# Optimization experiments

Measured on AMD Instinct MI355X. Metric: run time of the kernel, lower is better.

The kernel has to match this reference:

```python
import jax, jax.numpy as jnp
import numpy as np

N_NODES = 50000
W_IN = 256
W_OUT = 256
HEADS = 8
D_HEAD = W_OUT // HEADS
NUM_EDGE = 3
N_EDGES = 800000
NEG_SLOPE = 0.2


def setup_inputs() -> dict:
    key = jax.random.key(0)
    ks = jax.random.split(key, 10)
    x = jax.random.normal(ks[0], (N_NODES, W_IN), dtype=jnp.float32)
    adj = jax.random.randint(ks[1], (NUM_EDGE, 2, N_EDGES), 0, N_NODES, dtype=jnp.int64)
    sw = 1.0 / np.sqrt(W_IN)
    # Per-edge-type GATConv params, stacked on leading edge-type axis
    Ws = jax.random.normal(ks[2], (NUM_EDGE, W_IN, HEADS * D_HEAD), dtype=jnp.float32) * sw
    a_l = jax.random.normal(ks[3], (NUM_EDGE, HEADS, D_HEAD), dtype=jnp.float32) * 0.1
    a_r = jax.random.normal(ks[4], (NUM_EDGE, HEADS, D_HEAD), dtype=jnp.float32) * 0.1
    bias = jnp.zeros((NUM_EDGE, HEADS * D_HEAD), dtype=jnp.float32)
    # Semantic attention layer: Linear(w_out -> 1)
    att_w = jax.random.normal(ks[5], (W_OUT, 1), dtype=jnp.float32) * (1.0 / np.sqrt(W_OUT))
    att_b = jnp.zeros((1,), dtype=jnp.float32)
    return {"x": x, "adj": adj, "Ws": Ws, "a_l": a_l, "a_r": a_r,
            "bias": bias, "att_w": att_w, "att_b": att_b}


def _gat(x, edge_index, W, al, ar, b):
    # x: [N, W_IN]; edge_index: [2, E]; W: [W_IN, H*D]; al/ar: [H, D]; b: [H*D]
    N = x.shape[0]
    h = (x @ W).reshape(N, HEADS, D_HEAD)            # [N, H, D]
    src, dst = edge_index[0], edge_index[1]
    el = jnp.einsum('nhd,hd->nh', h, al)             # src-side scores [N, H]
    er = jnp.einsum('nhd,hd->nh', h, ar)             # dst-side scores [N, H]
    e = jax.nn.leaky_relu(el[src] + er[dst], NEG_SLOPE)   # [E, H]
    # segment softmax over incoming edges of each dst node
    m = jax.ops.segment_max(e, dst, num_segments=N)       # [N, H]
    e = jnp.exp(e - m[dst])
    s = jax.ops.segment_sum(e, dst, num_segments=N)       # [N, H]
    alpha = e / (s[dst] + 1e-9)                           # [E, H]
    out = jax.ops.segment_sum(alpha[:, :, None] * h[src], dst, num_segments=N)
    return out.reshape(N, HEADS * D_HEAD) + b             # concat heads [N, W_OUT]


def reference(x, adj, Ws, a_l, a_r, bias, att_w, att_b):
    outs = [_gat(x, adj[i], Ws[i], a_l[i], a_r[i], bias[i]) for i in range(NUM_EDGE)]
    stacked = jnp.stack(outs, axis=1)                     # [N, T, W_OUT]
    # AttentionLayer: scores = Linear(stacked) viewed as [N, 1, T]; NO softmax (faithful)
    att = (stacked @ att_w + att_b).reshape(-1, 1, NUM_EDGE)  # [N, 1, T]
    return jnp.matmul(att, stacked).squeeze(1)            # [N, W_OUT]
```

## Files before the change

kernel.cpp:

```cpp
#include <hip/hip_runtime.h>

#define N_NODES 50000
#define W_IN    256
#define W_OUT   256
#define HEADS   8
#define NUM_T   3
#define N_EDGES 800000
#define NEG_SLOPE 0.2f

#define NB      128
#define BSH     9
#define BNODES  512
#define P1_EPT  16
#define P1_CHUNK (256 * P1_EPT)
#define P1_BLOCKS ((N_EDGES + P1_CHUNK - 1) / P1_CHUNK)
#define NB_USED ((N_NODES + BNODES - 1) / BNODES)

#define MT_BLOCKS ((N_NODES + 127) / 128)
#define GATHER_BLOCKS ((N_NODES + 3) / 4)

#if defined(__has_builtin)
#if __has_builtin(__builtin_amdgcn_global_load_lds)
#define HAS_GLL 1
#endif
#endif

typedef __attribute__((ext_vector_type(8))) short bf16x8;
typedef __attribute__((ext_vector_type(4))) float f32x4;

__device__ __forceinline__ unsigned short f2b(float f) {
    unsigned u = __float_as_uint(f);
    u = (u + 0x7fffu + ((u >> 16) & 1u)) >> 16;
    return (unsigned short)u;
}
__device__ __forceinline__ float blo(unsigned u) { return __uint_as_float(u << 16); }
__device__ __forceinline__ float bhi(unsigned u) { return __uint_as_float(u & 0xffff0000u); }

__global__ __launch_bounds__(256) void convert_x(const float* __restrict__ x,
                                                 unsigned short* __restrict__ xb) {
    const size_t i = ((size_t)blockIdx.x * 256 + threadIdx.x) * 4;
    const float4 v = *(const float4*)(x + i);
    ushort4 o;
    o.x = f2b(v.x); o.y = f2b(v.y); o.z = f2b(v.z); o.w = f2b(v.w);
    *(ushort4*)(xb + i) = o;
}

__global__ __launch_bounds__(256) void convert_W(const float* __restrict__ Wsrc,
                                                 unsigned short* __restrict__ Wt) {
    const int t = blockIdx.y;
    const int gid = blockIdx.x * 256 + threadIdx.x;
    const int k = gid >> 8, n = gid & 255;
    Wt[(size_t)t * 65536 + (size_t)n * 256 + k] = f2b(Wsrc[(size_t)t * 65536 + gid]);
}

__global__ __launch_bounds__(256) void p1_hist(const int* __restrict__ adj,
                                               int* __restrict__ bucket_cnt) {
    __shared__ int lh[NB];
    const int t = blockIdx.y;
    const int tid = threadIdx.x;
    if (tid < NB) lh[tid] = 0;
    __syncthreads();

    const int* dstp = adj + (size_t)t * 2 * N_EDGES + N_EDGES;
    const int e0 = blockIdx.x * P1_CHUNK + tid * P1_EPT;
#pragma unroll
    for (int i = 0; i < P1_EPT; ++i) {
        const int e = e0 + i;
        if (e < N_EDGES) atomicAdd(&lh[dstp[e] >> BSH], 1);
    }
    __syncthreads();
    if (tid < NB && lh[tid] > 0) atomicAdd(&bucket_cnt[t * NB + tid], lh[tid]);
}

__global__ __launch_bounds__(128) void p1_scan(const int* __restrict__ bucket_cnt,
                                               int* __restrict__ bucket_ptr,
                                               int* __restrict__ bucket_cur) {
    __shared__ int s[NB];
    const int tid = threadIdx.x;
    for (int t = 0; t < NUM_T; ++t) {
        const int v = bucket_cnt[t * NB + tid];
        s[tid] = v;
        __syncthreads();
        for (int off = 1; off < NB; off <<= 1) {
            int o = (tid >= off) ? s[tid - off] : 0;
            __syncthreads();
            s[tid] += o;
            __syncthreads();
        }
        const int incl = s[tid];
        const int excl = incl - v;
        bucket_ptr[t * (NB + 1) + tid] = excl;
        bucket_cur[t * NB + tid] = excl;
        if (tid == NB - 1) bucket_ptr[t * (NB + 1) + NB] = incl;
        __syncthreads();
    }
}

__global__ __launch_bounds__(256) void p1_scatter(const int* __restrict__ adj,
                                                  int* __restrict__ bucket_cur,
                                                  uint2* __restrict__ part) {
    __shared__ int lh[NB];
    __shared__ int loff[NB];
    __shared__ int lbase[NB];
    __shared__ uint2 buf[P1_CHUNK];
    const int t = blockIdx.y;
    const int tid = threadIdx.x;
    const int lane = tid & 63;
    const int wave = tid >> 6;
    if (tid < NB) lh[tid] = 0;
    __syncthreads();

    const int* srcp = adj + (size_t)t * 2 * N_EDGES;
    const int* dstp = srcp + N_EDGES;
    const int e0 = blockIdx.x * P1_CHUNK + tid * P1_EPT;

    int es[P1_EPT], ed[P1_EPT], rk[P1_EPT];
#pragma unroll
    for (int i = 0; i < P1_EPT; ++i) {
        const int e = e0 + i;
        if (e < N_EDGES) {
            es[i] = srcp[e];
            ed[i] = dstp[e];
            rk[i] = atomicAdd(&lh[ed[i] >> BSH], 1);
        } else {
            ed[i] = -1;
        }
    }
    __syncthreads();

    if (tid < NB && lh[tid] > 0)
        lbase[tid] = atomicAdd(&bucket_cur[t * NB + tid], lh[tid]);
    if (wave == 0) {
        const int c0 = lh[lane * 2], c1 = lh[lane * 2 + 1];
        const int s = c0 + c1;
        int run = s;
        for (int off = 1; off < 64; off <<= 1) {
            const int o = __shfl_up(run, off);
            if (lane >= off) run += o;
        }
        const int base = run - s;
        loff[lane * 2] = base;
        loff[lane * 2 + 1] = base + c0;
    }
    __syncthreads();

#pragma unroll
    for (int i = 0; i < P1_EPT; ++i)
        if (ed[i] >= 0)
            buf[loff[ed[i] >> BSH] + rk[i]] =
                make_uint2((unsigned)es[i], (unsigned)ed[i]);
    __syncthreads();

    uint2* pt = part + (size_t)t * N_EDGES;
    int nvalid = N_EDGES - blockIdx.x * P1_CHUNK;
    if (nvalid > P1_CHUNK) nvalid = P1_CHUNK;
    for (int idx = tid; idx < nvalid; idx += 256) {
        const uint2 e = buf[idx];
        const int b = (int)(e.y >> BSH);
        pt[lbase[b] + (idx - loff[b])] = e;
    }
}

__global__ __launch_bounds__(256) void p2_csr(const uint2* __restrict__ part,
                                              const int* __restrict__ bucket_ptr,
                                              int* __restrict__ row_ptr_all,
                                              int* __restrict__ csr_all) {
    __shared__ int sc[BNODES];
    const int b = blockIdx.x;
    const int t = blockIdx.y;
    const int tid = threadIdx.x;
    const int lane = tid & 63;
    const int wave = tid >> 6;

    const uint2* pt = part + (size_t)t * N_EDGES;
    int* row_ptr = row_ptr_all + (size_t)t * (N_NODES + 1);
    int* csr = csr_all + (size_t)t * N_EDGES;

    const int bp0 = bucket_ptr[t * (NB + 1) + b];
    const int bp1 = bucket_ptr[t * (NB + 1) + b + 1];
    const int node0 = b * BNODES;
    int nn = N_NODES - node0; if (nn > BNODES) nn = BNODES;

    sc[tid] = 0; sc[tid + 256] = 0;
    __syncthreads();

    for (int idx = bp0 + tid; idx < bp1; idx += 256)
        atomicAdd(&sc[pt[idx].y - node0], 1);
    __syncthreads();

    if (wave == 0) {
        int v[8], ex[8];
        int s = 0;
#pragma unroll
        for (int i = 0; i < 8; ++i) { v[i] = sc[lane * 8 + i]; ex[i] = s; s += v[i]; }
        int run = s;
        for (int off = 1; off < 64; off <<= 1) {
            int o = __shfl_up(run, off);
            if (lane >= off) run += o;
        }
        const int base = run - s;
#pragma unroll
        for (int i = 0; i < 8; ++i) sc[lane * 8 + i] = base + ex[i];
    }
    __syncthreads();

    for (int i = tid; i < nn; i += 256) row_ptr[node0 + i] = bp0 + sc[i];
    if (b == NB_USED - 1 && tid == 0) row_ptr[N_NODES] = N_EDGES;
    __syncthreads();

    for (int idx = bp0 + tid; idx < bp1; idx += 256) {
        const uint2 e = pt[idx];
        const int pos = bp0 + atomicAdd(&sc[e.y - node0], 1);
        csr[pos] = (int)e.x;
    }
}

__global__ __launch_bounds__(256) void gemm_fused(const unsigned short* __restrict__ xb,
                                                  const unsigned short* __restrict__ Wt,
                                                  unsigned short* __restrict__ H) {
    __shared__ __attribute__((aligned(16))) unsigned short As[128 * 32];
    __shared__ __attribute__((aligned(16))) unsigned short Bs[128 * 32];

    const int tid  = threadIdx.x;
    const int wave = tid >> 6;
    const int lane = tid & 63;
    const int quad = lane >> 4;
    const int l16  = lane & 15;

    const int m0 = blockIdx.x * 128;
    const int n0 = blockIdx.y * 128;
    const int t  = blockIdx.z;

    const unsigned short* Bt = Wt + (size_t)t * 65536 + (size_t)n0 * W_IN;
    unsigned short* Hc = H + (size_t)t * N_NODES * W_OUT;

    const int moff = (wave >> 1) * 64;
    const int noff = (wave & 1) * 64;

    f32x4 acc[4][4] = {};

    const int srow = tid >> 2;
    const int sch  = (tid & 3) * 8;
    int ar0 = m0 + srow;       if (ar0 > N_NODES - 1) ar0 = N_NODES - 1;
    int ar1 = m0 + 64 + srow;  if (ar1 > N_NODES - 1) ar1 = N_NODES - 1;
    const unsigned short* a0p = xb + (size_t)ar0 * W_IN + sch;
    const unsigned short* a1p = xb + (size_t)ar1 * W_IN + sch;
    const unsigned short* b0p = Bt + (size_t)srow * W_IN + sch;
    const unsigned short* b1p = Bt + (size_t)(64 + srow) * W_IN + sch;
#if defined(HAS_GLL)
    const int ldso0 = wave * 64 * 8;
    const int ldso1 = (256 + wave * 64) * 8;
#endif

    for (int k0 = 0; k0 < W_IN; k0 += 32) {
#if defined(HAS_GLL)
        __builtin_amdgcn_global_load_lds(
            (const __attribute__((address_space(1))) void*)(a0p + k0),
            (__attribute__((address_space(3))) void*)(As + ldso0), 16, 0, 0);
        __builtin_amdgcn_global_load_lds(
            (const __attribute__((address_space(1))) void*)(a1p + k0),
            (__attribute__((address_space(3))) void*)(As + ldso1), 16, 0, 0);
        __builtin_amdgcn_global_load_lds(
            (const __attribute__((address_space(1))) void*)(b0p + k0),
            (__attribute__((address_space(3))) void*)(Bs + ldso0), 16, 0, 0);
        __builtin_amdgcn_global_load_lds(
            (const __attribute__((address_space(1))) void*)(b1p + k0),
            (__attribute__((address_space(3))) void*)(Bs + ldso1), 16, 0, 0);
#else
        {
            const uint4 av0 = *(const uint4*)(a0p + k0);
            const uint4 av1 = *(const uint4*)(a1p + k0);
            const uint4 bv0 = *(const uint4*)(b0p + k0);
            const uint4 bv1 = *(const uint4*)(b1p + k0);
            *(uint4*)&As[(size_t)tid * 8] = av0;
            *(uint4*)&As[2048 + (size_t)tid * 8] = av1;
            *(uint4*)&Bs[(size_t)tid * 8] = bv0;
            *(uint4*)&Bs[2048 + (size_t)tid * 8] = bv1;
        }
#endif
        __syncthreads();

        bf16x8 af[4], bfr[4];
#pragma unroll
        for (int mi = 0; mi < 4; ++mi)
            af[mi] = *(const bf16x8*)&As[(moff + mi * 16 + l16) * 32 + quad * 8];
#pragma unroll
        for (int ni = 0; ni < 4; ++ni)
            bfr[ni] = *(const bf16x8*)&Bs[(noff + ni * 16 + l16) * 32 + quad * 8];
#pragma unroll
        for (int mi = 0; mi < 4; ++mi)
#pragma unroll
            for (int ni = 0; ni < 4; ++ni)
                acc[mi][ni] = __builtin_amdgcn_mfma_f32_16x16x32_bf16(
                    af[mi], bfr[ni], acc[mi][ni], 0, 0, 0);
        __syncthreads();
    }

#pragma unroll
    for (int mi = 0; mi < 4; ++mi)
#pragma unroll
        for (int reg = 0; reg < 4; ++reg) {
            const int gr = m0 + moff + mi * 16 + quad * 4 + reg;
            if (gr < N_NODES)
#pragma unroll
                for (int ni = 0; ni < 4; ++ni)
                    Hc[(size_t)gr * W_OUT + n0 + noff + ni * 16 + l16] =
                        f2b(acc[mi][ni][reg]);
        }
}

__global__ __launch_bounds__(256) void compute_elr(
    const unsigned short* __restrict__ H, const float* __restrict__ a_l,
    const float* __restrict__ a_r, float* __restrict__ el,
    float* __restrict__ er) {
    const int node = (blockIdx.x * blockDim.x + threadIdx.x) >> 6;
    if (node >= N_NODES) return;
    const int t = blockIdx.y;
    const int lane = threadIdx.x & 63;
    const int h = lane >> 3;
    const int j8 = lane & 7;

    const size_t row = (size_t)t * N_NODES + node;
    const uint2 u = *(const uint2*)(H + row * W_OUT + h * 32 + j8 * 4);
    const float4 av = *(const float4*)(a_l + t * 256 + h * 32 + j8 * 4);
    const float4 rv = *(const float4*)(a_r + t * 256 + h * 32 + j8 * 4);
    const float c0 = blo(u.x), c1 = bhi(u.x), c2 = blo(u.y), c3 = bhi(u.y);
    float pl = c0 * av.x + c1 * av.y + c2 * av.z + c3 * av.w;
    float pr = c0 * rv.x + c1 * rv.y + c2 * rv.z + c3 * rv.w;
#pragma unroll
    for (int off = 1; off < 8; off <<= 1) {
        pl += __shfl_xor(pl, off);
        pr += __shfl_xor(pr, off);
    }
    if (j8 == 0) el[row * HEADS + h] = pl;
    if (j8 == 1) er[row * HEADS + h] = pr;
}

__device__ __forceinline__ void gather_accum(const int node, const int lane,
                                             const int* __restrict__ csr_src,
                                             const int* __restrict__ row_ptr,
                                             const float* __restrict__ el,
                                             const float* __restrict__ er,
                                             const unsigned short* __restrict__ H,
                                             float2 (&acc)[4], float& ssum) {
    const int half = lane >> 5;
    const int d8 = lane & 31;
    const int hh = d8 >> 2;

    const int beg = row_ptr[node];
    const int deg = row_ptr[node + 1] - beg;
    if (deg <= 0) return;
    const float erv = er[(size_t)node * HEADS + hh];

    int mysrc = (lane < deg) ? csr_src[beg + lane] : 0;
    const int npairs = (deg + 1) >> 1;

    int src0 = __shfl(mysrc, half);
    uint4 u0 = *(const uint4*)(H + (size_t)src0 * W_OUT + d8 * 8);
    float elv0 = el[(size_t)src0 * HEADS + hh];

    for (int q = 0; q < npairs; ++q) {
        int src1 = 0; uint4 u1 = u0; float elv1 = 0.f;
        const int q1 = q + 1;
        if (q1 < npairs) {
            if ((q1 & 31) == 0) {
                const int cb = beg + (q1 >> 5) * 64;
                mysrc = (cb + lane < beg + deg) ? csr_src[cb + lane] : 0;
            }
            src1 = __shfl(mysrc, (2 * q1 + half) & 63);
            u1 = *(const uint4*)(H + (size_t)src1 * W_OUT + d8 * 8);
            elv1 = el[(size_t)src1 * HEADS + hh];
        }
        float v = elv0 + erv;
        v = (v > 0.f) ? v : NEG_SLOPE * v;
        const float w = (2 * q + half < deg) ? __expf(v) : 0.f;
        acc[0].x += w * blo(u0.x); acc[0].y += w * bhi(u0.x);
        acc[1].x += w * blo(u0.y); acc[1].y += w * bhi(u0.y);
        acc[2].x += w * blo(u0.z); acc[2].y += w * bhi(u0.z);
        acc[3].x += w * blo(u0.w); acc[3].y += w * bhi(u0.w);
        ssum += w;
        src0 = src1; u0 = u1; elv0 = elv1;
    }
}

__global__ __launch_bounds__(256) void gat_gather_all(
    const int* __restrict__ csr_src, const int* __restrict__ row_ptr,
    const float* __restrict__ el, const float* __restrict__ er,
    const unsigned short* __restrict__ H,
    const float* __restrict__ bias, const float* __restrict__ att_w,
    const float* __restrict__ att_b, float* __restrict__ out) {
    const int node = (blockIdx.x * blockDim.x + threadIdx.x) >> 6;
    const int lane = threadIdx.x & 63;
    if (node >= N_NODES) return;

    float2 acc[NUM_T][4] = {};
    float ssum[NUM_T] = {};

#pragma unroll
    for (int t = 0; t < NUM_T; ++t)
        gather_accum(node, lane,
                     csr_src + (size_t)t * N_EDGES,
                     row_ptr + (size_t)t * (N_NODES + 1),
                     el + (size_t)t * N_NODES * HEADS,
                     er + (size_t)t * N_NODES * HEADS,
                     H + (size_t)t * N_NODES * W_OUT,
                     acc[t], ssum[t]);

#pragma unroll
    for (int t = 0; t < NUM_T; ++t) {
#pragma unroll
        for (int i = 0; i < 4; ++i) {
            acc[t][i].x += __shfl_xor(acc[t][i].x, 32);
            acc[t][i].y += __shfl_xor(acc[t][i].y, 32);
        }
        ssum[t] += __shfl_xor(ssum[t], 32);
    }

    const int half = lane >> 5;
    const int d8 = lane & 31;
    if (half == 0) {
        const float4 aw0 = *(const float4*)(att_w + d8 * 8);
        const float4 aw1 = *(const float4*)(att_w + d8 * 8 + 4);
        float h[NUM_T][8];
        float p[NUM_T];
#pragma unroll
        for (int t = 0; t < NUM_T; ++t) {
            const float inv = 1.f / (ssum[t] + 1e-9f);
            const float4 b0 = *(const float4*)(bias + t * W_OUT + d8 * 8);
            const float4 b1 = *(const float4*)(bias + t * W_OUT + d8 * 8 + 4);
            h[t][0] = acc[t][0].x * inv + b0.x;
            h[t][1] = acc[t][0].y * inv + b0.y;
            h[t][2] = acc[t][1].x * inv + b0.z;
            h[t][3] = acc[t][1].y * inv + b0.w;
            h[t][4] = acc[t][2].x * inv + b1.x;
            h[t][5] = acc[t][2].y * inv + b1.y;
            h[t][6] = acc[t][3].x * inv + b1.z;
            h[t][7] = acc[t][3].y * inv + b1.w;
            p[t] = h[t][0] * aw0.x + h[t][1] * aw0.y + h[t][2] * aw0.z +
                   h[t][3] * aw0.w + h[t][4] * aw1.x + h[t][5] * aw1.y +
                   h[t][6] * aw1.z + h[t][7] * aw1.w;
        }
#pragma unroll
        for (int off = 1; off < 32; off <<= 1) {
            p[0] += __shfl_xor(p[0], off);
            p[1] += __shfl_xor(p[1], off);
            p[2] += __shfl_xor(p[2], off);
        }
        const float ab = att_b[0];
        const float a0 = p[0] + ab, a1 = p[1] + ab, a2 = p[2] + ab;
        float4 o0, o1;
        o0.x = a0 * h[0][0] + a1 * h[1][0] + a2 * h[2][0];
        o0.y = a0 * h[0][1] + a1 * h[1][1] + a2 * h[2][1];
        o0.z = a0 * h[0][2] + a1 * h[1][2] + a2 * h[2][2];
        o0.w = a0 * h[0][3] + a1 * h[1][3] + a2 * h[2][3];
        o1.x = a0 * h[0][4] + a1 * h[1][4] + a2 * h[2][4];
        o1.y = a0 * h[0][5] + a1 * h[1][5] + a2 * h[2][5];
        o1.z = a0 * h[0][6] + a1 * h[1][6] + a2 * h[2][6];
        o1.w = a0 * h[0][7] + a1 * h[1][7] + a2 * h[2][7];
        *(float4*)(out + (size_t)node * W_OUT + d8 * 8) = o0;
        *(float4*)(out + (size_t)node * W_OUT + d8 * 8 + 4) = o1;
    }
}

extern "C" void kernel_launch(void* const* d_in, const int* in_sizes, int n_in,
                              void* d_out, int out_size, void* d_ws, size_t ws_size,
                              hipStream_t stream) {
    const float* x     = (const float*)d_in[0];
    const int*   adj   = (const int*)d_in[1];
    const float* Ws    = (const float*)d_in[2];
    const float* a_l   = (const float*)d_in[3];
    const float* a_r   = (const float*)d_in[4];
    const float* bias  = (const float*)d_in[5];
    const float* att_w = (const float*)d_in[6];
    const float* att_b = (const float*)d_in[7];
    float* out = (float*)d_out;

    char* w = (char*)d_ws;
    unsigned short* xb = (unsigned short*)w; w += (size_t)N_NODES * W_IN * 2;
    unsigned short* H  = (unsigned short*)w; w += (size_t)NUM_T * N_NODES * W_OUT * 2;
    unsigned short* Wt = (unsigned short*)w; w += (size_t)NUM_T * 65536 * 2;
    float* el = (float*)w; w += (size_t)NUM_T * N_NODES * HEADS * 4;
    float* er = (float*)w; w += (size_t)NUM_T * N_NODES * HEADS * 4;
    int* csr_src = (int*)w; w += (size_t)NUM_T * N_EDGES * 4;
    int* row_ptr = (int*)w; w += (size_t)NUM_T * (N_NODES + 1) * 4;
    int* bucket_cnt = (int*)w; w += NUM_T * NB * 4;
    int* bucket_ptr = (int*)w; w += NUM_T * (NB + 1) * 4;
    int* bucket_cur = (int*)w; w += NUM_T * NB * 4;
    uint2* part = (uint2*)H;

    hipMemsetAsync(bucket_cnt, 0, NUM_T * NB * sizeof(int), stream);
    convert_x<<<12500, 256, 0, stream>>>(x, xb);
    convert_W<<<dim3(256, NUM_T), 256, 0, stream>>>(Ws, Wt);
    p1_hist<<<dim3(P1_BLOCKS, NUM_T), 256, 0, stream>>>(adj, bucket_cnt);
    p1_scan<<<1, 128, 0, stream>>>(bucket_cnt, bucket_ptr, bucket_cur);
    p1_scatter<<<dim3(P1_BLOCKS, NUM_T), 256, 0, stream>>>(adj, bucket_cur, part);
    p2_csr<<<dim3(NB_USED, NUM_T), 256, 0, stream>>>(part, bucket_ptr, row_ptr,
                                                     csr_src);

    gemm_fused<<<dim3(MT_BLOCKS, 2, NUM_T), 256, 0, stream>>>(xb, Wt, H);

    compute_elr<<<dim3(GATHER_BLOCKS, NUM_T), 256, 0, stream>>>(H, a_l, a_r,
                                                                el, er);

    gat_gather_all<<<GATHER_BLOCKS, 256, 0, stream>>>(
        csr_src, row_ptr, el, er, H, bias, att_w, att_b, out);
}
```

Measured before the change: 462.8 us.

## Split gather into channel-half blocks with bf16 intermediate and separate combine kernel

The fused gather-plus-attention kernel is split in two. The gather kernel now handles half of the 256 channels per block, with four edge lanes per wave, and writes bf16 per-type outputs to a new workspace buffer. A separate combine kernel adds bias, computes the semantic attention scores and writes the final output. The aim is to shrink each wave's per-edge row footprint and raise parallelism and L2 locality over the channel halves. The cost is an extra kernel launch, a bf16 round-trip through global memory and some precision loss.

```diff
diff --git a/kernel.cpp b/kernel.cpp
--- a/kernel.cpp
+++ b/kernel.cpp
@@ -18,6 +18,7 @@
 
 #define MT_BLOCKS ((N_NODES + 127) / 128)
 #define GATHER_BLOCKS ((N_NODES + 3) / 4)
+#define SPLIT_BLOCKS 25000
 
 #if defined(__has_builtin)
 #if __has_builtin(__builtin_amdgcn_global_load_lds)
@@ -336,130 +337,139 @@
     if (j8 == 1) er[row * HEADS + h] = pr;
 }
 
-__device__ __forceinline__ void gather_accum(const int node, const int lane,
-                                             const int* __restrict__ csr_src,
-                                             const int* __restrict__ row_ptr,
-                                             const float* __restrict__ el,
-                                             const float* __restrict__ er,
-                                             const unsigned short* __restrict__ H,
-                                             float2 (&acc)[4], float& ssum) {
-    const int half = lane >> 5;
-    const int d8 = lane & 31;
-    const int hh = d8 >> 2;
-
-    const int beg = row_ptr[node];
-    const int deg = row_ptr[node + 1] - beg;
-    if (deg <= 0) return;
-    const float erv = er[(size_t)node * HEADS + hh];
-
-    int mysrc = (lane < deg) ? csr_src[beg + lane] : 0;
-    const int npairs = (deg + 1) >> 1;
-
-    int src0 = __shfl(mysrc, half);
-    uint4 u0 = *(const uint4*)(H + (size_t)src0 * W_OUT + d8 * 8);
-    float elv0 = el[(size_t)src0 * HEADS + hh];
-
-    for (int q = 0; q < npairs; ++q) {
-        int src1 = 0; uint4 u1 = u0; float elv1 = 0.f;
-        const int q1 = q + 1;
-        if (q1 < npairs) {
-            if ((q1 & 31) == 0) {
-                const int cb = beg + (q1 >> 5) * 64;
-                mysrc = (cb + lane < beg + deg) ? csr_src[cb + lane] : 0;
-            }
-            src1 = __shfl(mysrc, (2 * q1 + half) & 63);
-            u1 = *(const uint4*)(H + (size_t)src1 * W_OUT + d8 * 8);
-            elv1 = el[(size_t)src1 * HEADS + hh];
-        }
-        float v = elv0 + erv;
-        v = (v > 0.f) ? v : NEG_SLOPE * v;
-        const float w = (2 * q + half < deg) ? __expf(v) : 0.f;
-        acc[0].x += w * blo(u0.x); acc[0].y += w * bhi(u0.x);
-        acc[1].x += w * blo(u0.y); acc[1].y += w * bhi(u0.y);
-        acc[2].x += w * blo(u0.z); acc[2].y += w * bhi(u0.z);
-        acc[3].x += w * blo(u0.w); acc[3].y += w * bhi(u0.w);
-        ssum += w;
-        src0 = src1; u0 = u1; elv0 = elv1;
-    }
-}
-
-__global__ __launch_bounds__(256) void gat_gather_all(
+__global__ __launch_bounds__(256) void gat_gather_split(
     const int* __restrict__ csr_src, const int* __restrict__ row_ptr,
     const float* __restrict__ el, const float* __restrict__ er,
-    const unsigned short* __restrict__ H,
-    const float* __restrict__ bias, const float* __restrict__ att_w,
-    const float* __restrict__ att_b, float* __restrict__ out) {
-    const int node = (blockIdx.x * blockDim.x + threadIdx.x) >> 6;
+    const unsigned short* __restrict__ H, unsigned short* __restrict__ ot) {
+    const int bid = blockIdx.x;
+    const int q   = bid >> 3;
+    const int r   = bid & 7;
+    const int ch  = r >> 2;
+    const int sub = r & 3;
+    const int node = (q * 4 + sub) * 4 + (threadIdx.x >> 6);
+    if (node >= N_NODES) return;
     const int lane = threadIdx.x & 63;
-    if (node >= N_NODES) return;
+    const int g    = lane >> 4;
+    const int d16  = lane & 15;
+    const int hh   = ch * 4 + (d16 >> 2);
+    const int cbase = ch * 128 + d16 * 8;
 
     float2 acc[NUM_T][4] = {};
     float ssum[NUM_T] = {};
 
 #pragma unroll
-    for (int t = 0; t < NUM_T; ++t)
-        gather_accum(node, lane,
-                     csr_src + (size_t)t * N_EDGES,
-                     row_ptr + (size_t)t * (N_NODES + 1),
-                     el + (size_t)t * N_NODES * HEADS,
-                     er + (size_t)t * N_NODES * HEADS,
-                     H + (size_t)t * N_NODES * W_OUT,
-                     acc[t], ssum[t]);
-
-#pragma unroll
     for (int t = 0; t < NUM_T; ++t) {
+        const int* cs = csr_src + (size_t)t * N_EDGES;
+        const int* rp = row_ptr + (size_t)t * (N_NODES + 1);
+        const float* elc = el + (size_t)t * N_NODES * HEADS;
+        const float* erc = er + (size_t)t * N_NODES * HEADS;
+        const unsigned short* Hc = H + (size_t)t * N_NODES * W_OUT;
+
+        const int beg = rp[node];
+        const int deg = rp[node + 1] - beg;
+        if (deg <= 0) continue;
+        const float erv = erc[(size_t)node * HEADS + hh];
+
+        int mysrc = (lane < deg) ? cs[beg + lane] : 0;
+        const int nq = (deg + 3) >> 2;
+
+        int s0 = __shfl(mysrc, g);
+        uint4 u0 = *(const uint4*)(Hc + (size_t)s0 * W_OUT + cbase);
+        float e0 = elc[(size_t)s0 * HEADS + hh];
+
+        for (int qd = 0; qd < nq; ++qd) {
+            int s1 = 0; uint4 u1 = u0; float e1 = 0.f;
+            const int q1 = qd + 1;
+            if (q1 < nq) {
+                if ((q1 & 15) == 0) {
+                    const int base = beg + (q1 >> 4) * 64;
+                    mysrc = (base + lane < beg + deg) ? cs[base + lane] : 0;
+                }
+                s1 = __shfl(mysrc, (4 * q1 + g) & 63);
+                u1 = *(const uint4*)(Hc + (size_t)s1 * W_OUT + cbase);
+                e1 = elc[(size_t)s1 * HEADS + hh];
+            }
+            float v = e0 + erv;
+            v = (v > 0.f) ? v : NEG_SLOPE * v;
+            const float w = (4 * qd + g < deg) ? __expf(v) : 0.f;
+            acc[t][0].x += w * blo(u0.x); acc[t][0].y += w * bhi(u0.x);
+            acc[t][1].x += w * blo(u0.y); acc[t][1].y += w * bhi(u0.y);
+            acc[t][2].x += w * blo(u0.z); acc[t][2].y += w * bhi(u0.z);
+            acc[t][3].x += w * blo(u0.w); acc[t][3].y += w * bhi(u0.w);
+            ssum[t] += w;
+            s0 = s1; u0 = u1; e0 = e1;
+        }
+    }
+
+#pragma unroll
+    for (int t = 0; t < NUM_T; ++t) {
 #pragma unroll
         for (int i = 0; i < 4; ++i) {
+            acc[t][i].x += __shfl_xor(acc[t][i].x, 16);
             acc[t][i].x += __shfl_xor(acc[t][i].x, 32);
+            acc[t][i].y += __shfl_xor(acc[t][i].y, 16);
             acc[t][i].y += __shfl_xor(acc[t][i].y, 32);
         }
+        ssum[t] += __shfl_xor(ssum[t], 16);
         ssum[t] += __shfl_xor(ssum[t], 32);
     }
 
-    const int half = lane >> 5;
-    const int d8 = lane & 31;
-    if (half == 0) {
-        const float4 aw0 = *(const float4*)(att_w + d8 * 8);
-        const float4 aw1 = *(const float4*)(att_w + d8 * 8 + 4);
-        float h[NUM_T][8];
-        float p[NUM_T];
+    if (g == 0) {
 #pragma unroll
         for (int t = 0; t < NUM_T; ++t) {
             const float inv = 1.f / (ssum[t] + 1e-9f);
-            const float4 b0 = *(const float4*)(bias + t * W_OUT + d8 * 8);
-            const float4 b1 = *(const float4*)(bias + t * W_OUT + d8 * 8 + 4);
-            h[t][0] = acc[t][0].x * inv + b0.x;
-            h[t][1] = acc[t][0].y * inv + b0.y;
-            h[t][2] = acc[t][1].x * inv + b0.z;
-            h[t][3] = acc[t][1].y * inv + b0.w;
-            h[t][4] = acc[t][2].x * inv + b1.x;
-            h[t][5] = acc[t][2].y * inv + b1.y;
-            h[t][6] = acc[t][3].x * inv + b1.z;
-            h[t][7] = acc[t][3].y * inv + b1.w;
-            p[t] = h[t][0] * aw0.x + h[t][1] * aw0.y + h[t][2] * aw0.z +
-                   h[t][3] * aw0.w + h[t][4] * aw1.x + h[t][5] * aw1.y +
-                   h[t][6] * aw1.z + h[t][7] * aw1.w;
-        }
-#pragma unroll
-        for (int off = 1; off < 32; off <<= 1) {
-            p[0] += __shfl_xor(p[0], off);
-            p[1] += __shfl_xor(p[1], off);
-            p[2] += __shfl_xor(p[2], off);
-        }
-        const float ab = att_b[0];
-        const float a0 = p[0] + ab, a1 = p[1] + ab, a2 = p[2] + ab;
-        float4 o0, o1;
-        o0.x = a0 * h[0][0] + a1 * h[1][0] + a2 * h[2][0];
-        o0.y = a0 * h[0][1] + a1 * h[1][1] + a2 * h[2][1];
-        o0.z = a0 * h[0][2] + a1 * h[1][2] + a2 * h[2][2];
-        o0.w = a0 * h[0][3] + a1 * h[1][3] + a2 * h[2][3];
-        o1.x = a0 * h[0][4] + a1 * h[1][4] + a2 * h[2][4];
-        o1.y = a0 * h[0][5] + a1 * h[1][5] + a2 * h[2][5];
-        o1.z = a0 * h[0][6] + a1 * h[1][6] + a2 * h[2][6];
-        o1.w = a0 * h[0][7] + a1 * h[1][7] + a2 * h[2][7];
-        *(float4*)(out + (size_t)node * W_OUT + d8 * 8) = o0;
-        *(float4*)(out + (size_t)node * W_OUT + d8 * 8 + 4) = o1;
-    }
+            unsigned short o8[8];
+            o8[0] = f2b(acc[t][0].x * inv); o8[1] = f2b(acc[t][0].y * inv);
+            o8[2] = f2b(acc[t][1].x * inv); o8[3] = f2b(acc[t][1].y * inv);
+            o8[4] = f2b(acc[t][2].x * inv); o8[5] = f2b(acc[t][2].y * inv);
+            o8[6] = f2b(acc[t][3].x * inv); o8[7] = f2b(acc[t][3].y * inv);
+            *(uint4*)(ot + ((size_t)t * N_NODES + node) * W_OUT + cbase) =
+                *(const uint4*)o8;
+        }
+    }
+}
+
+__global__ __launch_bounds__(256) void combine(const unsigned short* __restrict__ ot,
+                                               const float* __restrict__ bias,
+                                               const float* __restrict__ att_w,
+                                               const float* __restrict__ att_b,
+                                               float* __restrict__ out) {
+    const int gw = (blockIdx.x * blockDim.x + threadIdx.x) >> 6;
+    const int lane = threadIdx.x & 63;
+    if (gw >= N_NODES) return;
+
+    const float4 aw = *(const float4*)(att_w + lane * 4);
+    const size_t base = (size_t)gw * W_OUT + lane * 4;
+    const size_t tstride = (size_t)N_NODES * W_OUT;
+
+    float4 v[NUM_T];
+    float p[NUM_T];
+#pragma unroll
+    for (int t = 0; t < NUM_T; ++t) {
+        const uint2 u = *(const uint2*)(ot + t * tstride + base);
+        const float4 bv = *(const float4*)(bias + t * W_OUT + lane * 4);
+        float4 hv;
+        hv.x = blo(u.x) + bv.x;
+        hv.y = bhi(u.x) + bv.y;
+        hv.z = blo(u.y) + bv.z;
+        hv.w = bhi(u.y) + bv.w;
+        v[t] = hv;
+        p[t] = hv.x * aw.x + hv.y * aw.y + hv.z * aw.z + hv.w * aw.w;
+    }
+#pragma unroll
+    for (int off = 1; off < 64; off <<= 1) {
+        p[0] += __shfl_xor(p[0], off);
+        p[1] += __shfl_xor(p[1], off);
+        p[2] += __shfl_xor(p[2], off);
+    }
+    const float ab = att_b[0];
+    const float a0 = p[0] + ab, a1 = p[1] + ab, a2 = p[2] + ab;
+    float4 o;
+    o.x = a0 * v[0].x + a1 * v[1].x + a2 * v[2].x;
+    o.y = a0 * v[0].y + a1 * v[1].y + a2 * v[2].y;
+    o.z = a0 * v[0].z + a1 * v[1].z + a2 * v[2].z;
+    o.w = a0 * v[0].w + a1 * v[1].w + a2 * v[2].w;
+    *(float4*)(out + base) = o;
 }
 
 extern "C" void kernel_launch(void* const* d_in, const int* in_sizes, int n_in,
@@ -479,6 +489,7 @@
     unsigned short* xb = (unsigned short*)w; w += (size_t)N_NODES * W_IN * 2;
     unsigned short* H  = (unsigned short*)w; w += (size_t)NUM_T * N_NODES * W_OUT * 2;
     unsigned short* Wt = (unsigned short*)w; w += (size_t)NUM_T * 65536 * 2;
+    unsigned short* ot = (unsigned short*)w; w += (size_t)NUM_T * N_NODES * W_OUT * 2;
     float* el = (float*)w; w += (size_t)NUM_T * N_NODES * HEADS * 4;
     float* er = (float*)w; w += (size_t)NUM_T * N_NODES * HEADS * 4;
     int* csr_src = (int*)w; w += (size_t)NUM_T * N_EDGES * 4;
@@ -486,7 +497,7 @@
     int* bucket_cnt = (int*)w; w += NUM_T * NB * 4;
     int* bucket_ptr = (int*)w; w += NUM_T * (NB + 1) * 4;
     int* bucket_cur = (int*)w; w += NUM_T * NB * 4;
-    uint2* part = (uint2*)H;
+    uint2* part = (uint2*)ot;
 
     hipMemsetAsync(bucket_cnt, 0, NUM_T * NB * sizeof(int), stream);
     convert_x<<<12500, 256, 0, stream>>>(x, xb);
@@ -502,6 +513,8 @@
     compute_elr<<<dim3(GATHER_BLOCKS, NUM_T), 256, 0, stream>>>(H, a_l, a_r,
                                                                 el, er);
 
-    gat_gather_all<<<GATHER_BLOCKS, 256, 0, stream>>>(
-        csr_src, row_ptr, el, er, H, bias, att_w, att_b, out);
-}
+    gat_gather_split<<<SPLIT_BLOCKS, 256, 0, stream>>>(
+        csr_src, row_ptr, el, er, H, ot);
+
+    combine<<<GATHER_BLOCKS, 256, 0, stream>>>(ot, bias, att_w, att_b, out);
+}
```

Result: slower. 503.8 us (+8.9%).

## Merge preprocessing, scan, GEMM and scatter launches into fewer fused heterogeneous kernels

Applied to the files above, without the earlier changes.

Cuts the launch count from nine (including a memset) to five. Conversion of x and W plus the edge histogram now share one kernel. The bucket scan runs as block 0 of the GEMM kernel, and the edge scatter runs alongside the el/er score computation. Each block's histogram is stored in a per-block matrix and turned into deterministic offsets by a serial column scan, which removes the global atomics and the bucket cursor. Because part now gets its own workspace instead of aliasing H, the stages can overlap, but the serial scan in one block may sit on the critical path of the GEMM kernel.

```diff
diff --git a/kernel.cpp b/kernel.cpp
--- a/kernel.cpp
+++ b/kernel.cpp
@@ -19,6 +19,16 @@
 #define MT_BLOCKS ((N_NODES + 127) / 128)
 #define GATHER_BLOCKS ((N_NODES + 3) / 4)
 
+#define PREP_CX   12500
+#define PREP_CW   768
+#define PREP_HIST (P1_BLOCKS * NUM_T)
+#define PREP_BLOCKS (PREP_CX + PREP_CW + PREP_HIST)
+
+#define SG_BLOCKS (1 + MT_BLOCKS * 2 * NUM_T)
+#define SE_SCAT   (P1_BLOCKS * NUM_T)
+#define SE_ELR    (GATHER_BLOCKS * NUM_T)
+#define SE_BLOCKS (SE_SCAT + SE_ELR)
+
 #if defined(__has_builtin)
 #if __has_builtin(__builtin_amdgcn_global_load_lds)
 #define HAS_GLL 1
@@ -36,200 +46,104 @@
 __device__ __forceinline__ float blo(unsigned u) { return __uint_as_float(u << 16); }
 __device__ __forceinline__ float bhi(unsigned u) { return __uint_as_float(u & 0xffff0000u); }
 
-__global__ __launch_bounds__(256) void convert_x(const float* __restrict__ x,
-                                                 unsigned short* __restrict__ xb) {
-    const size_t i = ((size_t)blockIdx.x * 256 + threadIdx.x) * 4;
-    const float4 v = *(const float4*)(x + i);
-    ushort4 o;
-    o.x = f2b(v.x); o.y = f2b(v.y); o.z = f2b(v.z); o.w = f2b(v.w);
-    *(ushort4*)(xb + i) = o;
-}
-
-__global__ __launch_bounds__(256) void convert_W(const float* __restrict__ Wsrc,
-                                                 unsigned short* __restrict__ Wt) {
-    const int t = blockIdx.y;
-    const int gid = blockIdx.x * 256 + threadIdx.x;
-    const int k = gid >> 8, n = gid & 255;
-    Wt[(size_t)t * 65536 + (size_t)n * 256 + k] = f2b(Wsrc[(size_t)t * 65536 + gid]);
-}
-
-__global__ __launch_bounds__(256) void p1_hist(const int* __restrict__ adj,
-                                               int* __restrict__ bucket_cnt) {
+__global__ __launch_bounds__(256) void prep(const float* __restrict__ x,
+                                            unsigned short* __restrict__ xb,
+                                            const float* __restrict__ Wsrc,
+                                            unsigned short* __restrict__ Wt,
+                                            const int* __restrict__ adj,
+                                            int* __restrict__ hist_mat) {
     __shared__ int lh[NB];
-    const int t = blockIdx.y;
+    const int b = blockIdx.x;
     const int tid = threadIdx.x;
+
+    if (b < PREP_CX) {
+        const size_t i = ((size_t)b * 256 + tid) * 4;
+        const float4 v = *(const float4*)(x + i);
+        ushort4 o;
+        o.x = f2b(v.x); o.y = f2b(v.y); o.z = f2b(v.z); o.w = f2b(v.w);
+        *(ushort4*)(xb + i) = o;
+        return;
+    }
+    if (b < PREP_CX + PREP_CW) {
+        const int idx = (b - PREP_CX) * 256 + tid;
+        const int t = idx >> 16;
+        const int gid = idx & 65535;
+        const int k = gid >> 8, n = gid & 255;
+        Wt[(size_t)t * 65536 + (size_t)n * 256 + k] =
+            f2b(Wsrc[(size_t)t * 65536 + gid]);
+        return;
+    }
+    const int hb = b - PREP_CX - PREP_CW;
+    const int t = hb / P1_BLOCKS;
+    const int c = hb % P1_BLOCKS;
     if (tid < NB) lh[tid] = 0;
     __syncthreads();
 
     const int* dstp = adj + (size_t)t * 2 * N_EDGES + N_EDGES;
-    const int e0 = blockIdx.x * P1_CHUNK + tid * P1_EPT;
+    const int e0 = c * P1_CHUNK + tid * P1_EPT;
 #pragma unroll
     for (int i = 0; i < P1_EPT; ++i) {
         const int e = e0 + i;
         if (e < N_EDGES) atomicAdd(&lh[dstp[e] >> BSH], 1);
     }
     __syncthreads();
-    if (tid < NB && lh[tid] > 0) atomicAdd(&bucket_cnt[t * NB + tid], lh[tid]);
-}
-
-__global__ __launch_bounds__(128) void p1_scan(const int* __restrict__ bucket_cnt,
-                                               int* __restrict__ bucket_ptr,
-                                               int* __restrict__ bucket_cur) {
-    __shared__ int s[NB];
-    const int tid = threadIdx.x;
-    for (int t = 0; t < NUM_T; ++t) {
-        const int v = bucket_cnt[t * NB + tid];
-        s[tid] = v;
-        __syncthreads();
-        for (int off = 1; off < NB; off <<= 1) {
-            int o = (tid >= off) ? s[tid - off] : 0;
-            __syncthreads();
-            s[tid] += o;
-            __syncthreads();
-        }
-        const int incl = s[tid];
-        const int excl = incl - v;
-        bucket_ptr[t * (NB + 1) + tid] = excl;
-        bucket_cur[t * NB + tid] = excl;
-        if (tid == NB - 1) bucket_ptr[t * (NB + 1) + NB] = incl;
-        __syncthreads();
-    }
-}
-
-__global__ __launch_bounds__(256) void p1_scatter(const int* __restrict__ adj,
-                                                  int* __restrict__ bucket_cur,
-                                                  uint2* __restrict__ part) {
-    __shared__ int lh[NB];
-    __shared__ int loff[NB];
-    __shared__ int lbase[NB];
-    __shared__ uint2 buf[P1_CHUNK];
-    const int t = blockIdx.y;
-    const int tid = threadIdx.x;
-    const int lane = tid & 63;
-    const int wave = tid >> 6;
-    if (tid < NB) lh[tid] = 0;
-    __syncthreads();
-
-    const int* srcp = adj + (size_t)t * 2 * N_EDGES;
-    const int* dstp = srcp + N_EDGES;
-    const int e0 = blockIdx.x * P1_CHUNK + tid * P1_EPT;
-
-    int es[P1_EPT], ed[P1_EPT], rk[P1_EPT];
-#pragma unroll
-    for (int i = 0; i < P1_EPT; ++i) {
-        const int e = e0 + i;
-        if (e < N_EDGES) {
-            es[i] = srcp[e];
-            ed[i] = dstp[e];
-            rk[i] = atomicAdd(&lh[ed[i] >> BSH], 1);
-        } else {
-            ed[i] = -1;
-        }
-    }
-    __syncthreads();
-
-    if (tid < NB && lh[tid] > 0)
-        lbase[tid] = atomicAdd(&bucket_cur[t * NB + tid], lh[tid]);
-    if (wave == 0) {
-        const int c0 = lh[lane * 2], c1 = lh[lane * 2 + 1];
-        const int s = c0 + c1;
-        int run = s;
-        for (int off = 1; off < 64; off <<= 1) {
-            const int o = __shfl_up(run, off);
-            if (lane >= off) run += o;
-        }
-        const int base = run - s;
-        loff[lane * 2] = base;
-        loff[lane * 2 + 1] = base + c0;
-    }
-    __syncthreads();
-
-#pragma unroll
-    for (int i = 0; i < P1_EPT; ++i)
-        if (ed[i] >= 0)
-            buf[loff[ed[i] >> BSH] + rk[i]] =
-                make_uint2((unsigned)es[i], (unsigned)ed[i]);
-    __syncthreads();
-
-    uint2* pt = part + (size_t)t * N_EDGES;
-    int nvalid = N_EDGES - blockIdx.x * P1_CHUNK;
-    if (nvalid > P1_CHUNK) nvalid = P1_CHUNK;
-    for (int idx = tid; idx < nvalid; idx += 256) {
-        const uint2 e = buf[idx];
-        const int b = (int)(e.y >> BSH);
-        pt[lbase[b] + (idx - loff[b])] = e;
-    }
-}
-
-__global__ __launch_bounds__(256) void p2_csr(const uint2* __restrict__ part,
-                                              const int* __restrict__ bucket_ptr,
-                                              int* __restrict__ row_ptr_all,
-                                              int* __restrict__ csr_all) {
-    __shared__ int sc[BNODES];
-    const int b = blockIdx.x;
-    const int t = blockIdx.y;
-    const int tid = threadIdx.x;
-    const int lane = tid & 63;
-    const int wave = tid >> 6;
-
-    const uint2* pt = part + (size_t)t * N_EDGES;
-    int* row_ptr = row_ptr_all + (size_t)t * (N_NODES + 1);
-    int* csr = csr_all + (size_t)t * N_EDGES;
-
-    const int bp0 = bucket_ptr[t * (NB + 1) + b];
-    const int bp1 = bucket_ptr[t * (NB + 1) + b + 1];
-    const int node0 = b * BNODES;
-    int nn = N_NODES - node0; if (nn > BNODES) nn = BNODES;
-
-    sc[tid] = 0; sc[tid + 256] = 0;
-    __syncthreads();
-
-    for (int idx = bp0 + tid; idx < bp1; idx += 256)
-        atomicAdd(&sc[pt[idx].y - node0], 1);
-    __syncthreads();
-
-    if (wave == 0) {
-        int v[8], ex[8];
-        int s = 0;
-#pragma unroll
-        for (int i = 0; i < 8; ++i) { v[i] = sc[lane * 8 + i]; ex[i] = s; s += v[i]; }
-        int run = s;
-        for (int off = 1; off < 64; off <<= 1) {
-            int o = __shfl_up(run, off);
-            if (lane >= off) run += o;
-        }
-        const int base = run - s;
-#pragma unroll
-        for (int i = 0; i < 8; ++i) sc[lane * 8 + i] = base + ex[i];
-    }
-    __syncthreads();
-
-    for (int i = tid; i < nn; i += 256) row_ptr[node0 + i] = bp0 + sc[i];
-    if (b == NB_USED - 1 && tid == 0) row_ptr[N_NODES] = N_EDGES;
-    __syncthreads();
-
-    for (int idx = bp0 + tid; idx < bp1; idx += 256) {
-        const uint2 e = pt[idx];
-        const int pos = bp0 + atomicAdd(&sc[e.y - node0], 1);
-        csr[pos] = (int)e.x;
-    }
-}
-
-__global__ __launch_bounds__(256) void gemm_fused(const unsigned short* __restrict__ xb,
-                                                  const unsigned short* __restrict__ Wt,
-                                                  unsigned short* __restrict__ H) {
+    if (tid < NB)
+        hist_mat[((size_t)t * P1_BLOCKS + c) * NB + tid] = lh[tid];
+}
+
+__global__ __launch_bounds__(256) void scan_gemm(int* __restrict__ hist_mat,
+                                                 int* __restrict__ bucket_ptr,
+                                                 const unsigned short* __restrict__ xb,
+                                                 const unsigned short* __restrict__ Wt,
+                                                 unsigned short* __restrict__ H) {
     __shared__ __attribute__((aligned(16))) unsigned short As[128 * 32];
     __shared__ __attribute__((aligned(16))) unsigned short Bs[128 * 32];
-
-    const int tid  = threadIdx.x;
+    const int tid = threadIdx.x;
+
+    if (blockIdx.x == 0) {
+        int* s = (int*)As;
+        for (int t = 0; t < NUM_T; ++t) {
+            int tot = 0;
+            if (tid < NB) {
+                int run = 0;
+                for (int c = 0; c < P1_BLOCKS; ++c) {
+                    const size_t ix = ((size_t)t * P1_BLOCKS + c) * NB + tid;
+                    const int v = hist_mat[ix];
+                    hist_mat[ix] = run;
+                    run += v;
+                }
+                tot = run;
+                s[tid] = tot;
+            }
+            __syncthreads();
+            for (int off = 1; off < NB; off <<= 1) {
+                int o = 0;
+                if (tid < NB && tid >= off) o = s[tid - off];
+                __syncthreads();
+                if (tid < NB) s[tid] += o;
+                __syncthreads();
+            }
+            if (tid < NB) {
+                bucket_ptr[t * (NB + 1) + tid] = s[tid] - tot;
+                if (tid == NB - 1) bucket_ptr[t * (NB + 1) + NB] = s[tid];
+            }
+            __syncthreads();
+        }
+        return;
+    }
+
+    const int g = blockIdx.x - 1;
+    const int mt = g % MT_BLOCKS;
+    const int nh = (g / MT_BLOCKS) & 1;
+    const int t  = g / (MT_BLOCKS * 2);
+
     const int wave = tid >> 6;
     const int lane = tid & 63;
     const int quad = lane >> 4;
     const int l16  = lane & 15;
 
-    const int m0 = blockIdx.x * 128;
-    const int n0 = blockIdx.y * 128;
-    const int t  = blockIdx.z;
+    const int m0 = mt * 128;
+    const int n0 = nh * 128;
 
     const unsigned short* Bt = Wt + (size_t)t * 65536 + (size_t)n0 * W_IN;
     unsigned short* Hc = H + (size_t)t * N_NODES * W_OUT;
@@ -309,31 +223,157 @@
         }
 }
 
-__global__ __launch_bounds__(256) void compute_elr(
+__global__ __launch_bounds__(256) void scatter_elr(
+    const int* __restrict__ adj, const int* __restrict__ bucket_ptr,
+    const int* __restrict__ hist_mat, uint2* __restrict__ part,
     const unsigned short* __restrict__ H, const float* __restrict__ a_l,
     const float* __restrict__ a_r, float* __restrict__ el,
     float* __restrict__ er) {
-    const int node = (blockIdx.x * blockDim.x + threadIdx.x) >> 6;
-    if (node >= N_NODES) return;
+    __shared__ int lh[NB];
+    __shared__ int loff[NB];
+    __shared__ int lbase[NB];
+    __shared__ uint2 buf[P1_CHUNK];
+    const int b = blockIdx.x;
+    const int tid = threadIdx.x;
+
+    if (b >= SE_SCAT) {
+        const int eb = b - SE_SCAT;
+        const int t = eb / GATHER_BLOCKS;
+        const int xbk = eb % GATHER_BLOCKS;
+        const int node = xbk * 4 + (tid >> 6);
+        if (node >= N_NODES) return;
+        const int lane = tid & 63;
+        const int h = lane >> 3;
+        const int j8 = lane & 7;
+
+        const size_t row = (size_t)t * N_NODES + node;
+        const uint2 u = *(const uint2*)(H + row * W_OUT + h * 32 + j8 * 4);
+        const float4 av = *(const float4*)(a_l + t * 256 + h * 32 + j8 * 4);
+        const float4 rv = *(const float4*)(a_r + t * 256 + h * 32 + j8 * 4);
+        const float c0 = blo(u.x), c1 = bhi(u.x), c2 = blo(u.y), c3 = bhi(u.y);
+        float pl = c0 * av.x + c1 * av.y + c2 * av.z + c3 * av.w;
+        float pr = c0 * rv.x + c1 * rv.y + c2 * rv.z + c3 * rv.w;
+#pragma unroll
+        for (int off = 1; off < 8; off <<= 1) {
+            pl += __shfl_xor(pl, off);
+            pr += __shfl_xor(pr, off);
+        }
+        if (j8 == 0) el[row * HEADS + h] = pl;
+        if (j8 == 1) er[row * HEADS + h] = pr;
+        return;
+    }
+
+    const int t = b / P1_BLOCKS;
+    const int c = b % P1_BLOCKS;
+    const int lane = tid & 63;
+    const int wave = tid >> 6;
+    if (tid < NB) lh[tid] = 0;
+    __syncthreads();
+
+    const int* srcp = adj + (size_t)t * 2 * N_EDGES;
+    const int* dstp = srcp + N_EDGES;
+    const int e0 = c * P1_CHUNK + tid * P1_EPT;
+
+    int es[P1_EPT], ed[P1_EPT], rk[P1_EPT];
+#pragma unroll
+    for (int i = 0; i < P1_EPT; ++i) {
+        const int e = e0 + i;
+        if (e < N_EDGES) {
+            es[i] = srcp[e];
+            ed[i] = dstp[e];
+            rk[i] = atomicAdd(&lh[ed[i] >> BSH], 1);
+        } else {
+            ed[i] = -1;
+        }
+    }
+    __syncthreads();
+
+    if (tid < NB)
+        lbase[tid] = bucket_ptr[t * (NB + 1) + tid] +
+                     hist_mat[((size_t)t * P1_BLOCKS + c) * NB + tid];
+    if (wave == 0) {
+        const int c0 = lh[lane * 2], c1 = lh[lane * 2 + 1];
+        const int s = c0 + c1;
+        int run = s;
+        for (int off = 1; off < 64; off <<= 1) {
+            const int o = __shfl_up(run, off);
+            if (lane >= off) run += o;
+        }
+        const int base = run - s;
+        loff[lane * 2] = base;
+        loff[lane * 2 + 1] = base + c0;
+    }
+    __syncthreads();
+
+#pragma unroll
+    for (int i = 0; i < P1_EPT; ++i)
+        if (ed[i] >= 0)
+            buf[loff[ed[i] >> BSH] + rk[i]] =
+                make_uint2((unsigned)es[i], (unsigned)ed[i]);
+    __syncthreads();
+
+    uint2* pt = part + (size_t)t * N_EDGES;
+    int nvalid = N_EDGES - c * P1_CHUNK;
+    if (nvalid > P1_CHUNK) nvalid = P1_CHUNK;
+    for (int idx = tid; idx < nvalid; idx += 256) {
+        const uint2 e = buf[idx];
+        const int bb = (int)(e.y >> BSH);
+        pt[lbase[bb] + (idx - loff[bb])] = e;
+    }
+}
+
+__global__ __launch_bounds__(256) void p2_csr(const uint2* __restrict__ part,
+                                              const int* __restrict__ bucket_ptr,
+                                              int* __restrict__ row_ptr_all,
+                                              int* __restrict__ csr_all) {
+    __shared__ int sc[BNODES];
+    const int b = blockIdx.x;
     const int t = blockIdx.y;
-    const int lane = threadIdx.x & 63;
-    const int h = lane >> 3;
-    const int j8 = lane & 7;
-
-    const size_t row = (size_t)t * N_NODES + node;
-    const uint2 u = *(const uint2*)(H + row * W_OUT + h * 32 + j8 * 4);
-    const float4 av = *(const float4*)(a_l + t * 256 + h * 32 + j8 * 4);
-    const float4 rv = *(const float4*)(a_r + t * 256 + h * 32 + j8 * 4);
-    const float c0 = blo(u.x), c1 = bhi(u.x), c2 = blo(u.y), c3 = bhi(u.y);
-    float pl = c0 * av.x + c1 * av.y + c2 * av.z + c3 * av.w;
-    float pr = c0 * rv.x + c1 * rv.y + c2 * rv.z + c3 * rv.w;
-#pragma unroll
-    for (int off = 1; off < 8; off <<= 1) {
-        pl += __shfl_xor(pl, off);
-        pr += __shfl_xor(pr, off);
-    }
-    if (j8 == 0) el[row * HEADS + h] = pl;
-    if (j8 == 1) er[row * HEADS + h] = pr;
+    const int tid = threadIdx.x;
+    const int lane = tid & 63;
+    const int wave = tid >> 6;
+
+    const uint2* pt = part + (size_t)t * N_EDGES;
+    int* row_ptr = row_ptr_all + (size_t)t * (N_NODES + 1);
+    int* csr = csr_all + (size_t)t * N_EDGES;
+
+    const int bp0 = bucket_ptr[t * (NB + 1) + b];
+    const int bp1 = bucket_ptr[t * (NB + 1) + b + 1];
+    const int node0 = b * BNODES;
+    int nn = N_NODES - node0; if (nn > BNODES) nn = BNODES;
+
+    sc[tid] = 0; sc[tid + 256] = 0;
+    __syncthreads();
+
+    for (int idx = bp0 + tid; idx < bp1; idx += 256)
+        atomicAdd(&sc[pt[idx].y - node0], 1);
+    __syncthreads();
+
+    if (wave == 0) {
+        int v[8], ex[8];
+        int s = 0;
+#pragma unroll
+        for (int i = 0; i < 8; ++i) { v[i] = sc[lane * 8 + i]; ex[i] = s; s += v[i]; }
+        int run = s;
+        for (int off = 1; off < 64; off <<= 1) {
+            int o = __shfl_up(run, off);
+            if (lane >= off) run += o;
+        }
+        const int base = run - s;
+#pragma unroll
+        for (int i = 0; i < 8; ++i) sc[lane * 8 + i] = base + ex[i];
+    }
+    __syncthreads();
+
+    for (int i = tid; i < nn; i += 256) row_ptr[node0 + i] = bp0 + sc[i];
+    if (b == NB_USED - 1 && tid == 0) row_ptr[N_NODES] = N_EDGES;
+    __syncthreads();
+
+    for (int idx = bp0 + tid; idx < bp1; idx += 256) {
+        const uint2 e = pt[idx];
+        const int pos = bp0 + atomicAdd(&sc[e.y - node0], 1);
+        csr[pos] = (int)e.x;
+    }
 }
 
 __device__ __forceinline__ void gather_accum(const int node, const int lane,
@@ -483,25 +523,16 @@
     float* er = (float*)w; w += (size_t)NUM_T * N_NODES * HEADS * 4;
     int* csr_src = (int*)w; w += (size_t)NUM_T * N_EDGES * 4;
     int* row_ptr = (int*)w; w += (size_t)NUM_T * (N_NODES + 1) * 4;
-    int* bucket_cnt = (int*)w; w += NUM_T * NB * 4;
+    uint2* part = (uint2*)w; w += (size_t)NUM_T * N_EDGES * 8;
+    int* hist_mat = (int*)w; w += (size_t)NUM_T * P1_BLOCKS * NB * 4;
     int* bucket_ptr = (int*)w; w += NUM_T * (NB + 1) * 4;
-    int* bucket_cur = (int*)w; w += NUM_T * NB * 4;
-    uint2* part = (uint2*)H;
-
-    hipMemsetAsync(bucket_cnt, 0, NUM_T * NB * sizeof(int), stream);
-    convert_x<<<12500, 256, 0, stream>>>(x, xb);
-    convert_W<<<dim3(256, NUM_T), 256, 0, stream>>>(Ws, Wt);
-    p1_hist<<<dim3(P1_BLOCKS, NUM_T), 256, 0, stream>>>(adj, bucket_cnt);
-    p1_scan<<<1, 128, 0, stream>>>(bucket_cnt, bucket_ptr, bucket_cur);
-    p1_scatter<<<dim3(P1_BLOCKS, NUM_T), 256, 0, stream>>>(adj, bucket_cur, part);
+
+    prep<<<PREP_BLOCKS, 256, 0, stream>>>(x, xb, Ws, Wt, adj, hist_mat);
+    scan_gemm<<<SG_BLOCKS, 256, 0, stream>>>(hist_mat, bucket_ptr, xb, Wt, H);
+    scatter_elr<<<SE_BLOCKS, 256, 0, stream>>>(adj, bucket_ptr, hist_mat, part,
+                                               H, a_l, a_r, el, er);
     p2_csr<<<dim3(NB_USED, NUM_T), 256, 0, stream>>>(part, bucket_ptr, row_ptr,
                                                      csr_src);
-
-    gemm_fused<<<dim3(MT_BLOCKS, 2, NUM_T), 256, 0, stream>>>(xb, Wt, H);
-
-    compute_elr<<<dim3(GATHER_BLOCKS, NUM_T), 256, 0, stream>>>(H, a_l, a_r,
-                                                                el, er);
-
     gat_gather_all<<<GATHER_BLOCKS, 256, 0, stream>>>(
         csr_src, row_ptr, el, er, H, bias, att_w, att_b, out);
 }
```

Result: no change. 457.9 us (-1.0%).
